# Kernel optimization log

Hardware: AMD Instinct MI355X
Metric: run time of the kernel (lower is better)

Reference implementation:

```python
import jax, jax.numpy as jnp
import numpy as np

N, FIN, C1, C2 = 4096, 6, 1000, 1000
K1, K2, KR = 3, 6, 3
NR, S, NCLS = 20, 205, 40


def pairwise_adj(x):
    # exp(-squared_euclidean_distance), RGCNN pairwise_distance
    inner = -2.0 * jnp.einsum('bnf,bmf->bnm', x, x)
    sq = jnp.sum(x * x, axis=-1, keepdims=True)
    return jnp.exp(-(sq + inner + jnp.swapaxes(sq, 1, 2)))


def knn_sparsify(adj, k):
    # keep top-k similarities per row, zero the rest (get_one_matrix_knn)
    vals, idx = jax.lax.top_k(adj, k)
    B, n, _ = adj.shape
    b = jnp.arange(B)[:, None, None]
    r = jnp.arange(n)[None, :, None]
    return jnp.zeros_like(adj).at[b, r, idx].set(vals)


def get_laplacian(W):
    # normalized Laplacian L = I - D^-1/2 W D^-1/2
    dinv = 1.0 / jnp.sqrt(jnp.sum(W, axis=-1))
    Lnorm = W * dinv[:, :, None] * dinv[:, None, :]
    return jnp.eye(W.shape[-1], dtype=W.dtype)[None] - Lnorm


def cheb_conv(x, L, W, b, K):
    # Chebyshev recursion: Tx0=x, Tx1=Lx, Txk=2L Tx_{k-1} - Tx_{k-2}
    Tx = [x]
    if K > 1:
        Tx.append(jnp.einsum('bnm,bmf->bnf', L, x))
    for _ in range(2, K):
        Tx.append(2.0 * jnp.einsum('bnm,bmf->bnf', L, Tx[-1]) - Tx[-2])
    xhat = jnp.concatenate(Tx, axis=-1)  # [B, N, K*Fin]
    return jnp.einsum('bnf,fo->bno', xhat, W) + b


def setup_inputs() -> dict:
    key = jax.random.key(0)
    ks = jax.random.split(key, 16)
    sc = 0.02
    return {
        'x': jax.random.normal(ks[0], (1, N, FIN), jnp.float32),
        'k': 40,
        'batch_size': 1,
        'num_points': N,
        'vertices_Reeb': jax.random.normal(ks[1], (NR, 3), jnp.float32),
        'laplacian_Reeb': jax.random.normal(ks[2], (NR, NR), jnp.float32),
        'sccs': jax.random.randint(ks[3], (NR, S), 0, N),
        'W1': jax.random.normal(ks[4], (K1 * FIN, C1), jnp.float32) * sc,
        'b1': jnp.zeros((C1,), jnp.float32),
        'W2': jax.random.normal(ks[5], (K2 * C1, C2), jnp.float32) * sc,
        'b2': jnp.zeros((C2,), jnp.float32),
        'Wr': jax.random.normal(ks[6], (KR * C1, C2), jnp.float32) * sc,
        'br': jnp.zeros((C2,), jnp.float32),
        'fc1_w': jax.random.normal(ks[7], (2 * C2, 512), jnp.float32) * sc,
        'fc1_b': jnp.zeros((512,), jnp.float32),
        'fc2_w': jax.random.normal(ks[8], (512, 128), jnp.float32) * sc,
        'fc2_b': jnp.zeros((128,), jnp.float32),
        'fc3_w': jax.random.normal(ks[9], (128, NCLS), jnp.float32) * sc,
        'fc3_b': jnp.zeros((NCLS,), jnp.float32),
    }


def reference(x, k, batch_size, num_points, vertices_Reeb, laplacian_Reeb, sccs,
              W1, b1, W2, b2, Wr, br, fc1_w, fc1_b, fc2_w, fc2_b, fc3_w, fc3_b):
    fro = lambda a: jnp.linalg.norm(a.reshape(-1))
    regs = []
    # dynamic KNN graph + Laplacian (no_grad in original -> stop_gradient)
    L = jax.lax.stop_gradient(get_laplacian(knn_sparsify(pairwise_adj(x), k)))
    out = jax.nn.relu(cheb_conv(x, L, W1, b1, K1))  # [1, N, 1000]
    regs.append(fro(jnp.einsum('bnc,bnm,bmf->bcf', out, L, x)))
    # Reeb pooling: max over each scc's node features (sample 0)
    vfr = jnp.max(out[0][sccs], axis=1)[None]  # [1, 20, 1000]
    L_reeb = laplacian_Reeb[None]
    # second dynamic graph on features
    L2 = jax.lax.stop_gradient(get_laplacian(knn_sparsify(pairwise_adj(out), k)))
    out2 = jax.nn.relu(cheb_conv(out, L2, W2, b2, K2))
    regs.append(fro(jnp.einsum('bnc,bnm,bmf->bcf', out2, L2, x)))
    out_reeb = jax.nn.relu(cheb_conv(vfr, L_reeb, Wr, br, KR))
    out_m = jnp.max(out2, axis=1)       # [1, 1000]
    reeb_m = jnp.max(out_reeb, axis=1)  # [1, 1000]
    of = jnp.concatenate([reeb_m, out_m], axis=1)  # [1, 2000]
    of = jax.nn.relu(of @ fc1_w + fc1_b)
    regs += [jnp.linalg.norm(fc1_w.T[0]) ** 2, fc1_b[0] ** 2]
    of = jax.nn.relu(of @ fc2_w + fc2_b)
    regs += [jnp.linalg.norm(fc2_w.T[0]) ** 2, fc2_b[0] ** 2]
    of = of @ fc3_w + fc3_b  # [1, 40]
    regs += [jnp.linalg.norm(fc3_w.T[0]) ** 2, fc3_b[0] ** 2]
    return of, jnp.stack(regs)
```

## Files before the change

### kernel.cpp

```cpp
#include <hip/hip_runtime.h>
#include <math.h>

#define N4    4096
#define FDIM  6
#define CC    1000
#define KP    1024
#define KP6   (6 * KP)
#define KNN   40
#define NRB   20
#define SSC   205

typedef __attribute__((ext_vector_type(8))) short bf16x8;
typedef __attribute__((ext_vector_type(4))) float f32x4;

__device__ __forceinline__ unsigned short f2bf(float f) {
    unsigned u = __float_as_uint(f);
    u = (u + 0x7fffu + ((u >> 16) & 1u)) >> 16;
    return (unsigned short)u;
}
__device__ __forceinline__ float bf2f(short s) {
    return __uint_as_float(((unsigned)(unsigned short)s) << 16);
}

__device__ __forceinline__ unsigned d2key(float d) {
    unsigned u = __float_as_uint(d);
    return ((int)u < 0) ? u : (~u) ^ 0x80000000u;
}
__device__ __forceinline__ float key2d(unsigned k) {
    unsigned u = (k >> 31) ? k : (~k) ^ 0x80000000u;
    return __uint_as_float(u);
}

__device__ __forceinline__ void gload16(const unsigned short* g, short* l) {
    __builtin_amdgcn_global_load_lds(
        (const __attribute__((address_space(1))) unsigned int*)g,
        (__attribute__((address_space(3))) unsigned int*)l, 16, 0, 0);
}


__global__ __launch_bounds__(256) void sqx_kernel(const float* __restrict__ x,
                                                  float* __restrict__ sq1,
                                                  float* __restrict__ xhat) {
    int n = blockIdx.x * blockDim.x + threadIdx.x;
    if (n >= N4) return;
    float s = 0.f;
#pragma unroll
    for (int f = 0; f < FDIM; ++f) {
        float v = x[n * FDIM + f];
        s += v * v;
        xhat[n * 18 + f] = v;
    }
    sq1[n] = s;
}


#define NHC 4
#define HSTRIDE 257

struct TopkSh {
    unsigned sv[N4];
    int hist[NHC * HSTRIDE];
    int sc[256];
    float red[8];
    unsigned short cidx[N4];
    unsigned short cv16[N4];
    unsigned s_pfx;
    int s_need, s_cnt, s_m;
};

__device__ __forceinline__ void topk_prep(TopkSh& sh, int t) {
    if (t == 0) { sh.s_pfx = 0u; sh.s_need = KNN; sh.s_cnt = 0; sh.s_m = 0; }
    for (int q = t; q < NHC * HSTRIDE; q += 512) sh.hist[q] = 0;
}

__device__ __forceinline__ void hist_pick(TopkSh& sh, int level, int t, int lane, int w, int nc) {
    if (t < 256) {
        int cnt = 0;
        for (int c = 0; c < nc; ++c) cnt += sh.hist[c * HSTRIDE + t];
        sh.sc[t] = cnt;
    }
    __syncthreads();
    if (w == 0) {
        int need = sh.s_need;
        unsigned pfx = sh.s_pfx;
        int c0 = sh.sc[4 * lane + 0], c1 = sh.sc[4 * lane + 1];
        int c2 = sh.sc[4 * lane + 2], c3 = sh.sc[4 * lane + 3];
        int s = c0 + c1 + c2 + c3;
        int suf = s;
#pragma unroll
        for (int off = 1; off < 64; off <<= 1) {
            int ov = __shfl_down(suf, off, 64);
            if (lane + off < 64) suf += ov;
        }
        int above = suf - s;
        int i3 = above + c3, i2 = i3 + c2, i1 = i2 + c1, i0 = i1 + c0;
        if (i3 >= need && i3 - c3 < need) { sh.s_need = need - (i3 - c3); sh.s_pfx = pfx | ((unsigned)(4 * lane + 3) << level); }
        if (i2 >= need && i2 - c2 < need) { sh.s_need = need - (i2 - c2); sh.s_pfx = pfx | ((unsigned)(4 * lane + 2) << level); }
        if (i1 >= need && i1 - c1 < need) { sh.s_need = need - (i1 - c1); sh.s_pfx = pfx | ((unsigned)(4 * lane + 1) << level); }
        if (i0 >= need && i0 - c0 < need) { sh.s_need = need - (i0 - c0); sh.s_pfx = pfx | ((unsigned)(4 * lane + 0) << level); }
    }
    __syncthreads();
}

template<int LASTLEVEL>
__device__ void topk_core(TopkSh& sh, int n, int* __restrict__ idx,
                          float* __restrict__ val, float* __restrict__ rowsum) {
    int t = threadIdx.x, lane = t & 63, w = t >> 6;
    __syncthreads();
    hist_pick(sh, 24, t, lane, w, NHC);
    unsigned b1 = sh.s_pfx >> 24;

    for (int i = t; i < N4; i += 512) {
        unsigned u = sh.sv[i];
        bool isc = ((u >> 24) >= b1);
        unsigned long long mm = __ballot(isc);
        int cw = __popcll(mm);
        int base = 0;
        if (lane == 0 && cw) base = atomicAdd(&sh.s_m, cw);
        base = __shfl(base, 0);
        if (isc) {
            int p = base + __popcll(mm & ((1ull << lane) - 1ull));
            sh.cidx[p] = (unsigned short)i;
            sh.cv16[p] = (unsigned short)(u >> 16);
        }
    }
    __syncthreads();
    int mcnt = sh.s_m;

    for (int q = t; q < HSTRIDE; q += 512) sh.hist[q] = 0;
    __syncthreads();
    {
        unsigned pb = sh.s_pfx >> 24;
        for (int j = t; j < mcnt; j += 512) {
            unsigned v = sh.cv16[j];
            if ((v >> 8) == pb) atomicAdd(&sh.hist[v & 255], 1);
        }
    }
    __syncthreads();
    hist_pick(sh, 16, t, lane, w, 1);

    if (LASTLEVEL == 0) {
        for (int q = t; q < HSTRIDE; q += 512) sh.hist[q] = 0;
        __syncthreads();
        {
            unsigned short p16 = (unsigned short)(sh.s_pfx >> 16);
            for (int j = t; j < mcnt; j += 512) {
                if (sh.cv16[j] == p16) {
                    unsigned u = sh.sv[sh.cidx[j]];
                    atomicAdd(&sh.hist[(u >> 8) & 255], 1);
                }
            }
        }
        __syncthreads();
        hist_pick(sh, 8, t, lane, w, 1);

        for (int q = t; q < HSTRIDE; q += 512) sh.hist[q] = 0;
        __syncthreads();
        {
            unsigned pfx = sh.s_pfx;
            unsigned short p16 = (unsigned short)(pfx >> 16);
            for (int j = t; j < mcnt; j += 512) {
                if (sh.cv16[j] == p16) {
                    unsigned u = sh.sv[sh.cidx[j]];
                    if ((u >> 8) == (pfx >> 8)) atomicAdd(&sh.hist[u & 255], 1);
                }
            }
        }
        __syncthreads();
        hist_pick(sh, 0, t, lane, w, 1);
    }

    unsigned Tbits = sh.s_pfx;
    if (LASTLEVEL == 16) Tbits |= (Tbits & 0x80000000u) ? 0u : 0xFFFFu;
    float Tf = __expf(-key2d(Tbits));
    int needEq = sh.s_need;

    float psum = 0.f;
    unsigned short T16 = (unsigned short)(Tbits >> 16);
    for (int j = t; j < mcnt; j += 512) {
        unsigned short v = sh.cv16[j];
        if (v >= T16) {
            unsigned u;
            if (LASTLEVEL == 16)
                u = ((unsigned)v << 16) | ((v & 0x8000u) ? 0u : 0xFFFFu);
            else
                u = sh.sv[sh.cidx[j]];
            if (u > Tbits) {
                int p = atomicAdd(&sh.s_cnt, 1);
                float fv = __expf(-key2d(u));
                idx[(size_t)n * KNN + p] = (int)sh.cidx[j];
                val[(size_t)n * KNN + p] = fv;
                psum += fv;
            }
        }
    }
#pragma unroll
    for (int o = 32; o; o >>= 1) psum += __shfl_down(psum, o);
    if (lane == 0) sh.red[w] = psum;
    __syncthreads();
    if (t == 0) {
        float s = 0.f;
#pragma unroll
        for (int q = 0; q < 8; ++q) s += sh.red[q];
        rowsum[n] = s + (float)needEq * Tf;
    }

    {
        int filled0 = KNN - needEq;
        int base_i = w * 512;
        int cnt = 0;
#pragma unroll
        for (int q = 0; q < 8; ++q) {
            bool eq = (sh.sv[base_i + q * 64 + lane] == Tbits);
            cnt += __popcll(__ballot(eq));
        }
        if (lane == 0) sh.sc[w] = cnt;
        __syncthreads();
        int pre = 0;
        for (int q = 0; q < w; ++q) pre += sh.sc[q];
        if (pre < needEq) {
            int run = pre;
            for (int q = 0; q < 8 && run < needEq; ++q) {
                bool eq = (sh.sv[base_i + q * 64 + lane] == Tbits);
                unsigned long long m = __ballot(eq);
                int lpre = __popcll(m & ((1ull << lane) - 1ull));
                if (eq && run + lpre < needEq) {
                    idx[(size_t)n * KNN + filled0 + run + lpre] = base_i + q * 64 + lane;
                    val[(size_t)n * KNN + filled0 + run + lpre] = Tf;
                }
                run += __popcll(m);
            }
        }
    }
}

__global__ __launch_bounds__(512) void topk_fused1(const float* __restrict__ x,
                                                   const float* __restrict__ sq1,
                                                   int* __restrict__ idx, float* __restrict__ val,
                                                   float* __restrict__ rowsum) {
    __shared__ TopkSh sh;
    __shared__ float xn[FDIM];
    __shared__ float sns;
    int n = blockIdx.x;
    int t = threadIdx.x;
    if (t < FDIM) xn[t] = x[n * FDIM + t];
    if (t == FDIM) sns = sq1[n];
    topk_prep(sh, t);
    __syncthreads();
    float x0 = xn[0], x1 = xn[1], x2 = xn[2], x3 = xn[3], x4 = xn[4], x5 = xn[5];
    float sn = sns;
    int* hw = &sh.hist[(t & 3) * HSTRIDE];
    unsigned prevb = 0xFFFFFFFFu; int rl = 0;
    for (int i = t; i < N4; i += 512) {
        const float2* xi = (const float2*)(x + i * FDIM);
        float2 p0 = xi[0], p1 = xi[1], p2 = xi[2];
        float d = x0 * p0.x + x1 * p0.y + x2 * p1.x + x3 * p1.y + x4 * p2.x + x5 * p2.y;
        float e = sn + sq1[i] - 2.f * d;
        unsigned k = d2key(e);
        sh.sv[i] = k;
        unsigned b = k >> 24;
        if (b == prevb) ++rl;
        else { if (rl) atomicAdd(&hw[prevb], rl); prevb = b; rl = 1; }
    }
    if (rl) atomicAdd(&hw[prevb], rl);
    topk_core<0>(sh, n, idx, val, rowsum);
}

__global__ __launch_bounds__(512) void topk_radix(const unsigned short* __restrict__ S,
                                                  int* __restrict__ idx, float* __restrict__ val,
                                                  float* __restrict__ rowsum) {
    __shared__ TopkSh sh;
    int n = blockIdx.x;
    int t = threadIdx.x;
    topk_prep(sh, t);
    const unsigned short* row = S + (size_t)n * N4;
    bf16x8 a = *(const bf16x8*)(row + 8 * t);
    __syncthreads();
    int* hw = &sh.hist[(t & 3) * HSTRIDE];
    unsigned prevb = 0xFFFFFFFFu; int rl = 0;
#pragma unroll
    for (int q = 0; q < 8; ++q) {
        unsigned k = d2key(bf2f(a[q]));
        sh.sv[8 * t + q] = k;
        unsigned b = k >> 24;
        if (b == prevb) ++rl;
        else { if (rl) atomicAdd(&hw[prevb], rl); prevb = b; rl = 1; }
    }
    if (rl) atomicAdd(&hw[prevb], rl);
    topk_core<16>(sh, n, idx, val, rowsum);
}

__global__ __launch_bounds__(256) void wnorm_kernel(float* __restrict__ wv,
                                                    const int* __restrict__ idx,
                                                    const float* __restrict__ rs) {
    int i = blockIdx.x * 256 + threadIdx.x;
    if (i >= N4 * KNN) return;
    int n = i / KNN;
    wv[i] = wv[i] * rsqrtf(rs[n]) * rsqrtf(rs[idx[i]]);
}

__global__ __launch_bounds__(64) void spmv_cheb(const float* __restrict__ Tc,
                                                const float* __restrict__ Tp,
                                                float* __restrict__ Tn,
                                                const int* __restrict__ idx,
                                                const float* __restrict__ wv,
                                                int F, int sC, int sP, int sN,
                                                float a, float b) {
    __shared__ int   si[KNN];
    __shared__ float sw[KNN];
    int n = blockIdx.x;
    if (threadIdx.x < KNN) {
        si[threadIdx.x] = idx[(size_t)n * KNN + threadIdx.x];
        sw[threadIdx.x] = wv[(size_t)n * KNN + threadIdx.x];
    }
    __syncthreads();
    for (int c = threadIdx.x; c < F; c += blockDim.x) {
        float s = 0.f;
#pragma unroll 8
        for (int j = 0; j < KNN; ++j) s += sw[j] * Tc[(size_t)si[j] * sC + c];
        float v = a * (Tc[(size_t)n * sC + c] - s);
        if (b != 0.f) v -= b * Tp[(size_t)n * sP + c];
        Tn[(size_t)n * sN + c] = v;
    }
}

__global__ __launch_bounds__(256) void spmv_cheb_bf(const unsigned short* __restrict__ Tcbf,
                                                    const unsigned short* __restrict__ Tpbf,
                                                    unsigned short* __restrict__ Tnbf,
                                                    const int* __restrict__ idx,
                                                    const float* __restrict__ wv,
                                                    float a, float b) {
    __shared__ int   si[KNN];
    __shared__ float sw[KNN];
    __shared__ float part[3][64][9];
    int n = blockIdx.x;
    int t = threadIdx.x;
    int tt = t & 63, g = t >> 6;
    if (t < KNN) {
        si[t] = idx[(size_t)n * KNN + t];
        sw[t] = wv[(size_t)n * KNN + t];
    }
    __syncthreads();
    int c = blockIdx.y * 512 + tt * 8;
    float acc0 = 0, acc1 = 0, acc2 = 0, acc3 = 0, acc4 = 0, acc5 = 0, acc6 = 0, acc7 = 0;
    int j0 = g * 10;
#pragma unroll
    for (int j = j0; j < j0 + 10; ++j) {
        bf16x8 v = *(const bf16x8*)(Tcbf + (size_t)si[j] * KP6 + c);
        float wj = sw[j];
        acc0 += wj * bf2f(v[0]); acc1 += wj * bf2f(v[1]);
        acc2 += wj * bf2f(v[2]); acc3 += wj * bf2f(v[3]);
        acc4 += wj * bf2f(v[4]); acc5 += wj * bf2f(v[5]);
        acc6 += wj * bf2f(v[6]); acc7 += wj * bf2f(v[7]);
    }
    if (g) {
        float* p = part[g - 1][tt];
        p[0] = acc0; p[1] = acc1; p[2] = acc2; p[3] = acc3;
        p[4] = acc4; p[5] = acc5; p[6] = acc6; p[7] = acc7;
    }
    __syncthreads();
    if (g == 0) {
#pragma unroll
        for (int pg = 0; pg < 3; ++pg) {
            const float* p = part[pg][tt];
            acc0 += p[0]; acc1 += p[1]; acc2 += p[2]; acc3 += p[3];
            acc4 += p[4]; acc5 += p[5]; acc6 += p[6]; acc7 += p[7];
        }
        bf16x8 tc = *(const bf16x8*)(Tcbf + (size_t)n * KP6 + c);
        float o0 = a * (bf2f(tc[0]) - acc0), o1 = a * (bf2f(tc[1]) - acc1);
        float o2 = a * (bf2f(tc[2]) - acc2), o3 = a * (bf2f(tc[3]) - acc3);
        float o4 = a * (bf2f(tc[4]) - acc4), o5 = a * (bf2f(tc[5]) - acc5);
        float o6 = a * (bf2f(tc[6]) - acc6), o7 = a * (bf2f(tc[7]) - acc7);
        if (b != 0.f) {
            bf16x8 tp = *(const bf16x8*)(Tpbf + (size_t)n * KP6 + c);
            o0 -= b * bf2f(tp[0]); o1 -= b * bf2f(tp[1]);
            o2 -= b * bf2f(tp[2]); o3 -= b * bf2f(tp[3]);
            o4 -= b * bf2f(tp[4]); o5 -= b * bf2f(tp[5]);
            o6 -= b * bf2f(tp[6]); o7 -= b * bf2f(tp[7]);
        }
        bf16x8 ob;
        ob[0] = (short)f2bf(o0); ob[1] = (short)f2bf(o1);
        ob[2] = (short)f2bf(o2); ob[3] = (short)f2bf(o3);
        ob[4] = (short)f2bf(o4); ob[5] = (short)f2bf(o5);
        ob[6] = (short)f2bf(o6); ob[7] = (short)f2bf(o7);
        *(bf16x8*)(Tnbf + (size_t)n * KP6 + c) = ob;
    }
}


__global__ __launch_bounds__(256) void cvt_bf16_kernel(const float* __restrict__ in,
                                                       unsigned short* __restrict__ out) {
    int i = blockIdx.x * 256 + threadIdx.x;
    int r = i >> 7, g = i & 127;
    bf16x8 v;
    if (g < 125) {
        float4 a = *(const float4*)(in + (size_t)r * CC + g * 8);
        float4 b = *(const float4*)(in + (size_t)r * CC + g * 8 + 4);
        v[0] = (short)f2bf(a.x); v[1] = (short)f2bf(a.y);
        v[2] = (short)f2bf(a.z); v[3] = (short)f2bf(a.w);
        v[4] = (short)f2bf(b.x); v[5] = (short)f2bf(b.y);
        v[6] = (short)f2bf(b.z); v[7] = (short)f2bf(b.w);
    } else {
#pragma unroll
        for (int q = 0; q < 8; ++q) v[q] = 0;
    }
    *(bf16x8*)(out + (size_t)r * KP6 + g * 8) = v;
}

__global__ __launch_bounds__(256) void w2t_kernel(const float* __restrict__ W2,
                                                  unsigned short* __restrict__ out) {
    __shared__ unsigned short tile[64][65];
    int t = threadIdx.x;
    int k0 = blockIdx.x * 64, n0 = blockIdx.y * 64, s = blockIdx.z;
#pragma unroll
    for (int p = 0; p < 16; ++p) {
        int i = p * 256 + t;
        int kk = i >> 6, nn = i & 63;
        int k = k0 + kk, n = n0 + nn;
        float v = (k < CC && n < CC) ? W2[((size_t)s * CC + k) * CC + n] : 0.f;
        tile[kk][nn] = f2bf(v);
    }
    __syncthreads();
#pragma unroll
    for (int p = 0; p < 16; ++p) {
        int i = p * 256 + t;
        int nn = i >> 6, kk = i & 63;
        out[(size_t)(n0 + nn) * KP6 + (size_t)s * KP + k0 + kk] = tile[kk][nn];
    }
}


#define LDT 32
#define SP2 136
#define SP 264
#define ABUF (128 * LDT)
#define BBUF (256 * LDT)

template<int STR>
__device__ __forceinline__ void gemm_core128_bk64(const unsigned short* __restrict__ Ag,
                                                  const unsigned short* __restrict__ Bg,
                                                  short* sm, int t,
                                                  int kbeg, int kend,
                                                  f32x4 (&acc)[4][4]) {
    int l = t & 63, w = t >> 6;
    int wm = (w >> 1) * 64, wn = (w & 1) * 64;
    int lr = l & 15, lq8 = (l >> 4) * 8;
    short* A0 = sm;
    short* A1 = sm + ABUF;
    short* B0 = sm + 2 * ABUF;
    short* B1 = sm + 3 * ABUF;
    size_t ga0 = (size_t)(32 * w + (l >> 2)) * STR + (l & 3) * 8;
    size_t ga1 = ga0 + (size_t)16 * STR;
    int lo = (32 * w) * LDT;
    for (int k0 = kbeg; k0 < kend; k0 += 64) {
        gload16(Ag + ga0 + k0,      A0 + lo);
        gload16(Ag + ga1 + k0,      A0 + lo + 16 * LDT);
        gload16(Ag + ga0 + k0 + 32, A1 + lo);
        gload16(Ag + ga1 + k0 + 32, A1 + lo + 16 * LDT);
        gload16(Bg + ga0 + k0,      B0 + lo);
        gload16(Bg + ga1 + k0,      B0 + lo + 16 * LDT);
        gload16(Bg + ga0 + k0 + 32, B1 + lo);
        gload16(Bg + ga1 + k0 + 32, B1 + lo + 16 * LDT);
        __syncthreads();
        bf16x8 af[4], bfr[4];
#pragma unroll
        for (int mi = 0; mi < 4; ++mi)
            af[mi] = *(const bf16x8*)&A0[(wm + mi * 16 + lr) * LDT + lq8];
#pragma unroll
        for (int ni = 0; ni < 4; ++ni)
            bfr[ni] = *(const bf16x8*)&B0[(wn + ni * 16 + lr) * LDT + lq8];
#pragma unroll
        for (int mi = 0; mi < 4; ++mi)
#pragma unroll
            for (int ni = 0; ni < 4; ++ni)
                acc[mi][ni] = __builtin_amdgcn_mfma_f32_16x16x32_bf16(af[mi], bfr[ni], acc[mi][ni], 0, 0, 0);
#pragma unroll
        for (int mi = 0; mi < 4; ++mi)
            af[mi] = *(const bf16x8*)&A1[(wm + mi * 16 + lr) * LDT + lq8];
#pragma unroll
        for (int ni = 0; ni < 4; ++ni)
            bfr[ni] = *(const bf16x8*)&B1[(wn + ni * 16 + lr) * LDT + lq8];
#pragma unroll
        for (int mi = 0; mi < 4; ++mi)
#pragma unroll
            for (int ni = 0; ni < 4; ++ni)
                acc[mi][ni] = __builtin_amdgcn_mfma_f32_16x16x32_bf16(af[mi], bfr[ni], acc[mi][ni], 0, 0, 0);
        __syncthreads();
    }
}

template<int STR>
__device__ __forceinline__ void gemm_core256(const unsigned short* __restrict__ Ag,
                                             const unsigned short* __restrict__ Bg,
                                             short* As, short* Bs, int t,
                                             int kbeg, int kend,
                                             f32x4 (&acc)[4][8]) {
    int l = t & 63, w = t >> 6;
    int wm = (w >> 1) * 64, wn = (w & 1) * 128;
    int lr = l & 15, lq8 = (l >> 4) * 8;
    size_t soff = (size_t)(16 * w + (l >> 2)) * STR + (l & 3) * 8;
    const unsigned short* gA = Ag + soff;
    const unsigned short* gB = Bg + soff;
    int wb = w * 512;
    gload16(gA + kbeg, As + wb);
    gload16(gA + kbeg + (size_t)64 * STR, As + wb + 64 * LDT);
    gload16(gB + kbeg, Bs + wb);
    gload16(gB + kbeg + (size_t)64 * STR, Bs + wb + 64 * LDT);
    gload16(gB + kbeg + (size_t)128 * STR, Bs + wb + 128 * LDT);
    gload16(gB + kbeg + (size_t)192 * STR, Bs + wb + 192 * LDT);
    __syncthreads();
    int cur = 0;
    for (int k0 = kbeg; k0 < kend; k0 += 32) {
        int nxt = cur ^ 1;
        if (k0 + 32 < kend) {
            short* nA = As + nxt * ABUF + wb;
            short* nB = Bs + nxt * BBUF + wb;
            gload16(gA + k0 + 32, nA);
            gload16(gA + k0 + 32 + (size_t)64 * STR, nA + 64 * LDT);
            gload16(gB + k0 + 32, nB);
            gload16(gB + k0 + 32 + (size_t)64 * STR, nB + 64 * LDT);
            gload16(gB + k0 + 32 + (size_t)128 * STR, nB + 128 * LDT);
            gload16(gB + k0 + 32 + (size_t)192 * STR, nB + 192 * LDT);
        }
        const short* cA = As + cur * ABUF;
        const short* cB = Bs + cur * BBUF;
        bf16x8 af[4], bfr[8];
#pragma unroll
        for (int mi = 0; mi < 4; ++mi)
            af[mi] = *(const bf16x8*)&cA[(wm + mi * 16 + lr) * LDT + lq8];
#pragma unroll
        for (int ni = 0; ni < 8; ++ni)
            bfr[ni] = *(const bf16x8*)&cB[(wn + ni * 16 + lr) * LDT + lq8];
#pragma unroll
        for (int mi = 0; mi < 4; ++mi)
#pragma unroll
            for (int ni = 0; ni < 8; ++ni)
                acc[mi][ni] = __builtin_amdgcn_mfma_f32_16x16x32_bf16(af[mi], bfr[ni], acc[mi][ni], 0, 0, 0);
        __syncthreads();
        cur = nxt;
    }
}

__global__ __launch_bounds__(256) void gemm_mfma_big(const unsigned short* __restrict__ A,
                                                     const unsigned short* __restrict__ B,
                                                     unsigned short* __restrict__ Cp) {
    __shared__ short smem[4 * ABUF];
    int t = threadIdx.x;
    int m0 = blockIdx.x * 128, n0 = blockIdx.y * 128;
    int kz = blockIdx.z;
    unsigned short* C = Cp + (size_t)kz * N4 * CC;
    f32x4 acc[4][4] = {};
    gemm_core128_bk64<KP6>(A + (size_t)m0 * KP6, B + (size_t)n0 * KP6, smem, t,
                           kz * 2 * KP, kz * 2 * KP + 2 * KP, acc);
    int l = t & 63, w = t >> 6;
    int wn = (w & 1) * 64;
    int lr = l & 15, lq4 = (l >> 4) * 4;
    int lrow = (w >> 1) * 16 + lq4;
#pragma unroll
    for (int mi = 0; mi < 4; ++mi) {
        __syncthreads();
#pragma unroll
        for (int ni = 0; ni < 4; ++ni) {
            int col = wn + ni * 16 + lr;
            f32x4 v = acc[mi][ni];
#pragma unroll
            for (int r = 0; r < 4; ++r) smem[(lrow + r) * SP2 + col] = (short)f2bf(v[r]);
        }
        __syncthreads();
#pragma unroll
        for (int q = 0; q < 2; ++q) {
            int row = q * 16 + (t >> 4);
            int col = (t & 15) * 8;
            int gm = m0 + (row >> 4) * 64 + mi * 16 + (row & 15);
            int gn = n0 + col;
            if (gn < CC) {
                bf16x8 vv = *(bf16x8*)&smem[row * SP2 + col];
                *(bf16x8*)(C + (size_t)gm * CC + gn) = vv;
            }
        }
    }
}

__global__ __launch_bounds__(256) void bias_relu_merge(const unsigned short* __restrict__ Cp,
                                                       const float* __restrict__ b2,
                                                       float* __restrict__ out2) {
    size_t i8 = (size_t)blockIdx.x * 256 + threadIdx.x;
    if (i8 >= (size_t)N4 * CC / 8) return;
    size_t i = i8 * 8;
    int c = (int)(i % CC);
    const size_t S = (size_t)N4 * CC;
    float s[8] = {};
#pragma unroll
    for (int z = 0; z < 3; ++z) {
        bf16x8 v = *(const bf16x8*)(Cp + z * S + i);
#pragma unroll
        for (int q = 0; q < 8; ++q) s[q] += bf2f(v[q]);
    }
    float4 o0, o1;
    o0.x = fmaxf(s[0] + b2[c + 0], 0.f); o0.y = fmaxf(s[1] + b2[c + 1], 0.f);
    o0.z = fmaxf(s[2] + b2[c + 2], 0.f); o0.w = fmaxf(s[3] + b2[c + 3], 0.f);
    o1.x = fmaxf(s[4] + b2[c + 4], 0.f); o1.y = fmaxf(s[5] + b2[c + 5], 0.f);
    o1.z = fmaxf(s[6] + b2[c + 6], 0.f); o1.w = fmaxf(s[7] + b2[c + 7], 0.f);
    *(float4*)(out2 + i) = o0;
    *(float4*)(out2 + i + 4) = o1;
}

__global__ __launch_bounds__(256, 2) void gram2_mfma(const unsigned short* __restrict__ Tall,
                                                     const float* __restrict__ sq2,
                                                     unsigned short* __restrict__ S) {
    __shared__ short smem[2 * ABUF + 2 * BBUF];
    short* As = smem;
    short* Bs = smem + 2 * ABUF;
    int t = threadIdx.x;
    int m0 = blockIdx.x * 128, n0 = blockIdx.y * 256;
    f32x4 acc[4][8] = {};
    gemm_core256<KP6>(Tall + (size_t)m0 * KP6, Tall + (size_t)n0 * KP6, As, Bs, t, 0, KP, acc);
    int l = t & 63, w = t >> 6;
    int wn = (w & 1) * 128;
    int lr = l & 15, lq4 = (l >> 4) * 4;
    int lrow = (w >> 1) * 16 + lq4;
#pragma unroll
    for (int mi = 0; mi < 4; ++mi) {
        __syncthreads();
        int mbase = m0 + (w >> 1) * 64 + mi * 16 + lq4;
#pragma unroll
        for (int ni = 0; ni < 8; ++ni) {
            int col = wn + ni * 16 + lr;
            float sn = sq2[n0 + col];
            f32x4 v = acc[mi][ni];
#pragma unroll
            for (int r = 0; r < 4; ++r)
                smem[(lrow + r) * SP + col] = (short)f2bf(sq2[mbase + r] + sn - 2.f * v[r]);
        }
        __syncthreads();
#pragma unroll
        for (int q = 0; q < 4; ++q) {
            int row = q * 8 + (t >> 5);
            int col = (t & 31) * 8;
            int gm = m0 + (row >> 4) * 64 + mi * 16 + (row & 15);
            int gn = n0 + col;
            bf16x8 vv = *(bf16x8*)&smem[row * SP + col];
            *(bf16x8*)(S + (size_t)gm * N4 + gn) = vv;
        }
    }
}


__global__ __launch_bounds__(256) void cheb1_out_kernel(const float* __restrict__ xhat,
                                                        const float* __restrict__ W1,
                                                        const float* __restrict__ b1,
                                                        float* __restrict__ outF) {
    __shared__ float xh[16][18];
    int n0 = blockIdx.x * 16;
    int tid = threadIdx.x;
    for (int i = tid; i < 16 * 18; i += 256) xh[i / 18][i % 18] = xhat[(size_t)n0 * 18 + i];
    __syncthreads();
    for (int c0 = 0; c0 < CC; c0 += 256) {
        int c = c0 + tid;
        if (c < CC) {
            float acc[16];
#pragma unroll
            for (int r = 0; r < 16; ++r) acc[r] = 0.f;
            for (int f = 0; f < 18; ++f) {
                float wv = W1[(size_t)f * CC + c];
#pragma unroll
                for (int r = 0; r < 16; ++r) acc[r] += xh[r][f] * wv;
            }
            float bb = b1[c];
#pragma unroll
            for (int r = 0; r < 16; ++r)
                outF[(size_t)(n0 + r) * CC + c] = fmaxf(acc[r] + bb, 0.f);
        }
    }
}


__global__ __launch_bounds__(256) void matT6_partial(const float* __restrict__ O,
                                                     const float* __restrict__ T, int ts,
                                                     float* __restrict__ M) {
    __shared__ float sT[128][6];
    int t = threadIdx.x;
    int c = blockIdx.x * 256 + t;
    int n0 = blockIdx.y * 128;
    for (int i = t; i < 128 * 6; i += 256) {
        int nn = i / 6, f = i % 6;
        sT[nn][f] = T[(size_t)(n0 + nn) * ts + f];
    }
    __syncthreads();
    if (c >= CC) return;
    float a0 = 0, a1 = 0, a2 = 0, a3 = 0, a4 = 0, a5 = 0;
    for (int nn = 0; nn < 128; ++nn) {
        float o = O[(size_t)(n0 + nn) * CC + c];
        a0 += o * sT[nn][0]; a1 += o * sT[nn][1]; a2 += o * sT[nn][2];
        a3 += o * sT[nn][3]; a4 += o * sT[nn][4]; a5 += o * sT[nn][5];
    }
    atomicAdd(&M[0 * CC + c], a0);
    atomicAdd(&M[1 * CC + c], a1);
    atomicAdd(&M[2 * CC + c], a2);
    atomicAdd(&M[3 * CC + c], a3);
    atomicAdd(&M[4 * CC + c], a4);
    atomicAdd(&M[5 * CC + c], a5);
}

__global__ __launch_bounds__(256) void fro_kernel(const float* __restrict__ M, float* __restrict__ dst) {
    __shared__ float red[256];
    int t = threadIdx.x;
    int i = blockIdx.x * 256 + t;
    float v = (i < 6 * CC) ? M[i] : 0.f;
    red[t] = v * v;
    __syncthreads();
    for (int o = 128; o; o >>= 1) { if (t < o) red[t] += red[t + o]; __syncthreads(); }
    if (t == 0) atomicAdd(dst, red[0]);
}


__global__ __launch_bounds__(256) void vfr_kernel(const float* __restrict__ outF,
                                                  const int* __restrict__ sccs,
                                                  float* __restrict__ vfr) {
    int r = blockIdx.y;
    int c = blockIdx.x * 256 + threadIdx.x;
    if (c >= CC) return;
    int s0 = blockIdx.z * 41;
    float m = 0.f;
    for (int s = s0; s < s0 + 41; ++s) {
        int n = sccs[r * SSC + s];
        m = fmaxf(m, outF[(size_t)n * CC + c]);
    }
    atomicMax((int*)&vfr[(size_t)r * CC + c], __float_as_int(m));
}

__global__ __launch_bounds__(256) void sq2_kernel(const float* __restrict__ outF,
                                                  float* __restrict__ sq2) {
    int lane = threadIdx.x & 63, w = threadIdx.x >> 6;
    int n = blockIdx.x * 4 + w;
    const float* row = outF + (size_t)n * CC;
    float s = 0.f;
    for (int i = lane; i < CC; i += 64) { float v = row[i]; s += v * v; }
#pragma unroll
    for (int o = 32; o; o >>= 1) s += __shfl_down(s, o);
    if (lane == 0) sq2[n] = s;
}

__global__ __launch_bounds__(256) void colmax_kernel(const float* __restrict__ O,
                                                     float* __restrict__ dst) {
    int c = blockIdx.x * 256 + threadIdx.x;
    if (c >= CC) return;
    int n0 = blockIdx.y * 64;
    float m = 0.f;
    for (int n = n0; n < n0 + 64; ++n) m = fmaxf(m, O[(size_t)n * CC + c]);
    atomicMax((int*)&dst[c], __float_as_int(m));
}


__global__ __launch_bounds__(256) void reeb_mm_kernel(const float* __restrict__ Lr,
                                                      const float* __restrict__ Vin,
                                                      const float* __restrict__ Vsub,
                                                      float* __restrict__ Vout, float a2) {
    int c = blockIdx.x * 256 + threadIdx.x;
    if (c >= CC) return;
    int r = blockIdx.y;
    float s = 0.f;
#pragma unroll
    for (int j = 0; j < NRB; ++j) s += Lr[r * NRB + j] * Vin[(size_t)j * CC + c];
    float v = a2 * s;
    if (Vsub) v -= Vsub[(size_t)r * CC + c];
    Vout[(size_t)r * CC + c] = v;
}

#define RKC 25
__global__ __launch_bounds__(256) void reeb_conv_splitk(const float* __restrict__ vfr,
                                                        const float* __restrict__ tr1,
                                                        const float* __restrict__ tr2,
                                                        const float* __restrict__ Wr,
                                                        float* __restrict__ rpre) {
    __shared__ float sA[NRB][RKC];
    int t = threadIdx.x;
    int kbase = blockIdx.y * RKC;
    for (int i = t; i < NRB * RKC; i += 256) {
        int r = i / RKC, kk = i % RKC;
        int kg = kbase + kk;
        float v;
        if (kg < CC)           v = vfr[(size_t)r * CC + kg];
        else if (kg < 2 * CC)  v = tr1[(size_t)r * CC + kg - CC];
        else                   v = tr2[(size_t)r * CC + kg - 2 * CC];
        sA[r][kk] = v;
    }
    __syncthreads();
    int c = blockIdx.x * 256 + t;
    if (c >= CC) return;
    float acc[NRB];
#pragma unroll
    for (int r = 0; r < NRB; ++r) acc[r] = 0.f;
    for (int kk = 0; kk < RKC; ++kk) {
        float wv = Wr[(size_t)(kbase + kk) * CC + c];
#pragma unroll
        for (int r = 0; r < NRB; ++r) acc[r] += sA[r][kk] * wv;
    }
#pragma unroll
    for (int r = 0; r < NRB; ++r) atomicAdd(&rpre[(size_t)r * CC + c], acc[r]);
}

__global__ __launch_bounds__(256) void reeb_max_kernel(const float* __restrict__ pre,
                                                       const float* __restrict__ br,
                                                       float* __restrict__ rbm) {
    int c = blockIdx.x * 256 + threadIdx.x;
    if (c >= CC) return;
    float bb = br[c];
    float m = 0.f;
    for (int r = 0; r < NRB; ++r) m = fmaxf(m, fmaxf(pre[(size_t)r * CC + c] + bb, 0.f));
    rbm[c] = m;
}


__global__ __launch_bounds__(256) void fc1_kernel(const float* __restrict__ rbm,
                                                  const float* __restrict__ otm,
                                                  const float* __restrict__ w,
                                                  float* __restrict__ h1pre) {
    int j = blockIdx.x * 256 + threadIdx.x;
    if (j >= 512) return;
    int i0 = blockIdx.y * 250;
    float s = 0.f;
    for (int i = i0; i < i0 + 250; ++i) {
        float v = (i < CC) ? rbm[i] : otm[i - CC];
        s += v * w[(size_t)i * 512 + j];
    }
    atomicAdd(&h1pre[j], s);
}

__global__ __launch_bounds__(512) void fc23_kernel(const float* __restrict__ h1pre,
                                                   const float* __restrict__ b1f,
                                                   const float* __restrict__ w2,
                                                   const float* __restrict__ b2f,
                                                   const float* __restrict__ w3,
                                                   const float* __restrict__ b3f,
                                                   float* __restrict__ dout) {
    __shared__ float h1[512];
    __shared__ float h2[128];
    int t = threadIdx.x;
    h1[t] = fmaxf(h1pre[t] + b1f[t], 0.f);
    __syncthreads();
    if (t < 128) {
        float s = b2f[t];
        for (int i = 0; i < 512; ++i) s += h1[i] * w2[(size_t)i * 128 + t];
        h2[t] = fmaxf(s, 0.f);
    }
    __syncthreads();
    if (t < 40) {
        float s = b3f[t];
        for (int i = 0; i < 128; ++i) s += h2[i] * w3[(size_t)i * 40 + t];
        dout[t] = s;
    }
}

__global__ __launch_bounds__(256) void finalize_kernel(const float* __restrict__ racc,
                                                       const float* __restrict__ f1w,
                                                       const float* __restrict__ f1b,
                                                       const float* __restrict__ f2w,
                                                       const float* __restrict__ f2b,
                                                       const float* __restrict__ f3w,
                                                       const float* __restrict__ f3b,
                                                       float* __restrict__ dout) {
    __shared__ float red[256];
    __shared__ float res[3];
    int t = threadIdx.x;
    float s1 = 0.f, s2 = 0.f, s3 = 0.f;
    for (int i = t; i < 2000; i += 256) { float v = f1w[(size_t)i * 512]; s1 += v * v; }
    for (int i = t; i < 512; i += 256) { float v = f2w[(size_t)i * 128]; s2 += v * v; }
    if (t < 128) { float v = f3w[(size_t)t * 40]; s3 = v * v; }

    red[t] = s1; __syncthreads();
    for (int o = 128; o; o >>= 1) { if (t < o) red[t] += red[t + o]; __syncthreads(); }
    if (t == 0) res[0] = red[0];
    __syncthreads();
    red[t] = s2; __syncthreads();
    for (int o = 128; o; o >>= 1) { if (t < o) red[t] += red[t + o]; __syncthreads(); }
    if (t == 0) res[1] = red[0];
    __syncthreads();
    red[t] = s3; __syncthreads();
    for (int o = 128; o; o >>= 1) { if (t < o) red[t] += red[t + o]; __syncthreads(); }
    if (t == 0) res[2] = red[0];
    __syncthreads();

    if (t == 0) {
        dout[40] = sqrtf(racc[0]);
        dout[41] = sqrtf(racc[1]);
        dout[42] = res[0];
        dout[43] = f1b[0] * f1b[0];
        dout[44] = res[1];
        dout[45] = f2b[0] * f2b[0];
        dout[46] = res[2];
        dout[47] = f3b[0] * f3b[0];
    }
}


extern "C" void kernel_launch(void* const* d_in, const int* in_sizes, int n_in,
                              void* d_out, int out_size, void* d_ws, size_t ws_size,
                              hipStream_t stream) {
    const float* x    = (const float*)d_in[0];
    const float* Lr   = (const float*)d_in[5];
    const int*   sccs = (const int*)d_in[6];
    const float* W1   = (const float*)d_in[7];
    const float* b1   = (const float*)d_in[8];
    const float* W2   = (const float*)d_in[9];
    const float* b2   = (const float*)d_in[10];
    const float* Wr   = (const float*)d_in[11];
    const float* br   = (const float*)d_in[12];
    const float* f1w  = (const float*)d_in[13];
    const float* f1b  = (const float*)d_in[14];
    const float* f2w  = (const float*)d_in[15];
    const float* f2b  = (const float*)d_in[16];
    const float* f3w  = (const float*)d_in[17];
    const float* f3b  = (const float*)d_in[18];
    float* dout = (float*)d_out;

    char* ws = (char*)d_ws;
    size_t off = 0;
    auto alloc = [&](size_t bytes) -> char* {
        char* p = ws + off;
        off = (off + bytes + 255) & ~(size_t)255;
        return p;
    };
    float* outF = (float*)alloc((size_t)N4 * CC * 4);
    unsigned short* Cpb = (unsigned short*)alloc((size_t)6 * N4 * CC * 2);
    unsigned short* Sb  = (unsigned short*)alloc((size_t)N4 * N4 * 2);
    unsigned short* Tall = (unsigned short*)alloc((size_t)N4 * KP6 * 2);
    unsigned short* W2T6 = Sb;
    float* xhat = (float*)alloc((size_t)N4 * 18 * 4);
    float* sq1  = (float*)alloc(N4 * 4);
    float* sq2  = (float*)alloc(N4 * 4);
    float* rs1  = (float*)alloc(N4 * 4);
    float* rs2  = (float*)alloc(N4 * 4);
    float* wv1  = (float*)alloc((size_t)N4 * KNN * 4);
    float* wv2  = (float*)alloc((size_t)N4 * KNN * 4);
    int*   ix1  = (int*)alloc((size_t)N4 * KNN * 4);
    int*   ix2  = (int*)alloc((size_t)N4 * KNN * 4);
    float* t2x  = (float*)alloc((size_t)N4 * FDIM * 4);
    float* tr1  = (float*)alloc((size_t)NRB * CC * 4);
    float* tr2  = (float*)alloc((size_t)NRB * CC * 4);
    char*  zbase = ws + off;
    float* Mb   = (float*)alloc(6 * CC * 4);
    float* Mb2  = (float*)alloc(6 * CC * 4);
    float* rbm  = (float*)alloc(CC * 4);
    float* otm  = (float*)alloc(CC * 4);
    float* h1p  = (float*)alloc(512 * 4);
    float* racc = (float*)alloc(64 * 4);
    float* rpre = (float*)alloc((size_t)NRB * CC * 4);
    float* vfr  = (float*)alloc((size_t)NRB * CC * 4);
    size_t zlen = (size_t)((ws + off) - zbase);
    if (off > ws_size) return;

    hipMemsetAsync(zbase, 0, zlen, stream);

    sqx_kernel<<<(N4 + 255) / 256, 256, 0, stream>>>(x, sq1, xhat);
    topk_fused1<<<N4, 512, 0, stream>>>(x, sq1, ix1, wv1, rs1);
    wnorm_kernel<<<(N4 * KNN + 255) / 256, 256, 0, stream>>>(wv1, ix1, rs1);

    spmv_cheb<<<N4, 64, 0, stream>>>(xhat, xhat, xhat + 6, ix1, wv1, FDIM, 18, 18, 18, 1.f, 0.f);
    spmv_cheb<<<N4, 64, 0, stream>>>(xhat + 6, xhat, xhat + 12, ix1, wv1, FDIM, 18, 18, 18, 2.f, 1.f);
    cheb1_out_kernel<<<N4 / 16, 256, 0, stream>>>(xhat, W1, b1, outF);

    matT6_partial<<<dim3(4, 32), 256, 0, stream>>>(outF, xhat + 6, 18, Mb);
    fro_kernel<<<24, 256, 0, stream>>>(Mb, racc + 0);

    vfr_kernel<<<dim3(4, NRB, 5), 256, 0, stream>>>(outF, sccs, vfr);

    sq2_kernel<<<N4 / 4, 256, 0, stream>>>(outF, sq2);
    cvt_bf16_kernel<<<N4 * 128 / 256, 256, 0, stream>>>(outF, Tall);
    gram2_mfma<<<dim3(N4 / 128, N4 / 256), 256, 0, stream>>>(Tall, sq2, Sb);
    topk_radix<<<N4, 512, 0, stream>>>(Sb, ix2, wv2, rs2);
    wnorm_kernel<<<(N4 * KNN + 255) / 256, 256, 0, stream>>>(wv2, ix2, rs2);

    w2t_kernel<<<dim3(16, 16, 6), 256, 0, stream>>>(W2, W2T6);

    spmv_cheb<<<N4, 64, 0, stream>>>(x, x, t2x, ix2, wv2, FDIM, FDIM, FDIM, FDIM, 1.f, 0.f);

    spmv_cheb_bf<<<dim3(N4, 2), 256, 0, stream>>>(Tall + 0 * KP, Tall + 0 * KP, Tall + 1 * KP, ix2, wv2, 1.f, 0.f);
    spmv_cheb_bf<<<dim3(N4, 2), 256, 0, stream>>>(Tall + 1 * KP, Tall + 0 * KP, Tall + 2 * KP, ix2, wv2, 2.f, 1.f);
    spmv_cheb_bf<<<dim3(N4, 2), 256, 0, stream>>>(Tall + 2 * KP, Tall + 1 * KP, Tall + 3 * KP, ix2, wv2, 2.f, 1.f);
    spmv_cheb_bf<<<dim3(N4, 2), 256, 0, stream>>>(Tall + 3 * KP, Tall + 2 * KP, Tall + 4 * KP, ix2, wv2, 2.f, 1.f);
    spmv_cheb_bf<<<dim3(N4, 2), 256, 0, stream>>>(Tall + 4 * KP, Tall + 3 * KP, Tall + 5 * KP, ix2, wv2, 2.f, 1.f);

    gemm_mfma_big<<<dim3(N4 / 128, 8, 3), 256, 0, stream>>>(Tall, W2T6, Cpb);
    bias_relu_merge<<<(int)(((size_t)N4 * CC / 8 + 255) / 256), 256, 0, stream>>>(Cpb, b2, outF);

    matT6_partial<<<dim3(4, 32), 256, 0, stream>>>(outF, t2x, FDIM, Mb2);
    fro_kernel<<<24, 256, 0, stream>>>(Mb2, racc + 1);

    colmax_kernel<<<dim3(4, 64), 256, 0, stream>>>(outF, otm);

    reeb_mm_kernel<<<dim3(4, NRB), 256, 0, stream>>>(Lr, vfr, nullptr, tr1, 1.f);
    reeb_mm_kernel<<<dim3(4, NRB), 256, 0, stream>>>(Lr, tr1, vfr, tr2, 2.f);
    reeb_conv_splitk<<<dim3(4, 120), 256, 0, stream>>>(vfr, tr1, tr2, Wr, rpre);
    reeb_max_kernel<<<4, 256, 0, stream>>>(rpre, br, rbm);

    fc1_kernel<<<dim3(2, 8), 256, 0, stream>>>(rbm, otm, f1w, h1p);
    fc23_kernel<<<1, 512, 0, stream>>>(h1p, f1b, f2w, f2b, f3w, f3b, dout);
    finalize_kernel<<<1, 256, 0, stream>>>(racc, f1w, f1b, f2w, f2b, f3w, f3b, dout);
}
```

Before: 604.6 us.

## Enlarge big GEMM tiles to 256x256 with 512 threads and split-K of four

The main MFMA GEMM moves from 128x128 tiles with 4 waves and a 3-way K split to 256x256 tiles with 8 waves and a 4-way K split. Each wave now computes 128x64 instead of 64x64. The goal is more operand reuse per byte loaded and fewer blocks. The merge kernel now sums four partial bf16 slices, which adds memory traffic and needs a larger partial buffer. The smaller grid may also leave the GPU less fully occupied.

Result: slower. 618.8 us (+2.3%).

```diff
diff --git a/kernel.cpp b/kernel.cpp
--- a/kernel.cpp
+++ b/kernel.cpp
@@ -435,59 +435,6 @@
 #define SP 264
 #define ABUF (128 * LDT)
 #define BBUF (256 * LDT)
-
-template<int STR>
-__device__ __forceinline__ void gemm_core128_bk64(const unsigned short* __restrict__ Ag,
-                                                  const unsigned short* __restrict__ Bg,
-                                                  short* sm, int t,
-                                                  int kbeg, int kend,
-                                                  f32x4 (&acc)[4][4]) {
-    int l = t & 63, w = t >> 6;
-    int wm = (w >> 1) * 64, wn = (w & 1) * 64;
-    int lr = l & 15, lq8 = (l >> 4) * 8;
-    short* A0 = sm;
-    short* A1 = sm + ABUF;
-    short* B0 = sm + 2 * ABUF;
-    short* B1 = sm + 3 * ABUF;
-    size_t ga0 = (size_t)(32 * w + (l >> 2)) * STR + (l & 3) * 8;
-    size_t ga1 = ga0 + (size_t)16 * STR;
-    int lo = (32 * w) * LDT;
-    for (int k0 = kbeg; k0 < kend; k0 += 64) {
-        gload16(Ag + ga0 + k0,      A0 + lo);
-        gload16(Ag + ga1 + k0,      A0 + lo + 16 * LDT);
-        gload16(Ag + ga0 + k0 + 32, A1 + lo);
-        gload16(Ag + ga1 + k0 + 32, A1 + lo + 16 * LDT);
-        gload16(Bg + ga0 + k0,      B0 + lo);
-        gload16(Bg + ga1 + k0,      B0 + lo + 16 * LDT);
-        gload16(Bg + ga0 + k0 + 32, B1 + lo);
-        gload16(Bg + ga1 + k0 + 32, B1 + lo + 16 * LDT);
-        __syncthreads();
-        bf16x8 af[4], bfr[4];
-#pragma unroll
-        for (int mi = 0; mi < 4; ++mi)
-            af[mi] = *(const bf16x8*)&A0[(wm + mi * 16 + lr) * LDT + lq8];
-#pragma unroll
-        for (int ni = 0; ni < 4; ++ni)
-            bfr[ni] = *(const bf16x8*)&B0[(wn + ni * 16 + lr) * LDT + lq8];
-#pragma unroll
-        for (int mi = 0; mi < 4; ++mi)
-#pragma unroll
-            for (int ni = 0; ni < 4; ++ni)
-                acc[mi][ni] = __builtin_amdgcn_mfma_f32_16x16x32_bf16(af[mi], bfr[ni], acc[mi][ni], 0, 0, 0);
-#pragma unroll
-        for (int mi = 0; mi < 4; ++mi)
-            af[mi] = *(const bf16x8*)&A1[(wm + mi * 16 + lr) * LDT + lq8];
-#pragma unroll
-        for (int ni = 0; ni < 4; ++ni)
-            bfr[ni] = *(const bf16x8*)&B1[(wn + ni * 16 + lr) * LDT + lq8];
-#pragma unroll
-        for (int mi = 0; mi < 4; ++mi)
-#pragma unroll
-            for (int ni = 0; ni < 4; ++ni)
-                acc[mi][ni] = __builtin_amdgcn_mfma_f32_16x16x32_bf16(af[mi], bfr[ni], acc[mi][ni], 0, 0, 0);
-        __syncthreads();
-    }
-}
 
 template<int STR>
 __device__ __forceinline__ void gemm_core256(const unsigned short* __restrict__ Ag,
@@ -541,40 +488,84 @@
     }
 }
 
-__global__ __launch_bounds__(256) void gemm_mfma_big(const unsigned short* __restrict__ A,
-                                                     const unsigned short* __restrict__ B,
-                                                     unsigned short* __restrict__ Cp) {
-    __shared__ short smem[4 * ABUF];
-    int t = threadIdx.x;
-    int m0 = blockIdx.x * 128, n0 = blockIdx.y * 128;
+__global__ __launch_bounds__(512, 2) void gemm_mfma_big(const unsigned short* __restrict__ A,
+                                                        const unsigned short* __restrict__ B,
+                                                        unsigned short* __restrict__ Cp) {
+    __shared__ short smem[4 * BBUF];
+    int t = threadIdx.x;
+    int m0 = blockIdx.x * 256, n0 = blockIdx.y * 256;
     int kz = blockIdx.z;
     unsigned short* C = Cp + (size_t)kz * N4 * CC;
-    f32x4 acc[4][4] = {};
-    gemm_core128_bk64<KP6>(A + (size_t)m0 * KP6, B + (size_t)n0 * KP6, smem, t,
-                           kz * 2 * KP, kz * 2 * KP + 2 * KP, acc);
+    f32x4 acc[8][4] = {};
     int l = t & 63, w = t >> 6;
-    int wn = (w & 1) * 64;
-    int lr = l & 15, lq4 = (l >> 4) * 4;
-    int lrow = (w >> 1) * 16 + lq4;
-#pragma unroll
-    for (int mi = 0; mi < 4; ++mi) {
+    int wm = (w >> 2) * 128, wn = (w & 3) * 64;
+    int lr = l & 15, lq8 = (l >> 4) * 8;
+    short* A0 = smem;
+    short* A1 = smem + BBUF;
+    short* B0 = smem + 2 * BBUF;
+    short* B1 = smem + 3 * BBUF;
+    const unsigned short* Ag = A + (size_t)m0 * KP6;
+    const unsigned short* Bg = B + (size_t)n0 * KP6;
+    size_t ga = (size_t)(32 * w + (l >> 2)) * KP6 + (l & 3) * 8;
+    int lo = (32 * w) * LDT;
+    int kbeg = kz * 1536, kend = kbeg + 1536;
+    for (int k0 = kbeg; k0 < kend; k0 += 64) {
+        gload16(Ag + ga + k0,                         A0 + lo);
+        gload16(Ag + ga + (size_t)16 * KP6 + k0,      A0 + lo + 16 * LDT);
+        gload16(Ag + ga + k0 + 32,                    A1 + lo);
+        gload16(Ag + ga + (size_t)16 * KP6 + k0 + 32, A1 + lo + 16 * LDT);
+        gload16(Bg + ga + k0,                         B0 + lo);
+        gload16(Bg + ga + (size_t)16 * KP6 + k0,      B0 + lo + 16 * LDT);
+        gload16(Bg + ga + k0 + 32,                    B1 + lo);
+        gload16(Bg + ga + (size_t)16 * KP6 + k0 + 32, B1 + lo + 16 * LDT);
+        __syncthreads();
+        bf16x8 af[8], bfr[4];
+#pragma unroll
+        for (int mi = 0; mi < 8; ++mi)
+            af[mi] = *(const bf16x8*)&A0[(wm + mi * 16 + lr) * LDT + lq8];
+#pragma unroll
+        for (int ni = 0; ni < 4; ++ni)
+            bfr[ni] = *(const bf16x8*)&B0[(wn + ni * 16 + lr) * LDT + lq8];
+#pragma unroll
+        for (int mi = 0; mi < 8; ++mi)
+#pragma unroll
+            for (int ni = 0; ni < 4; ++ni)
+                acc[mi][ni] = __builtin_amdgcn_mfma_f32_16x16x32_bf16(af[mi], bfr[ni], acc[mi][ni], 0, 0, 0);
+#pragma unroll
+        for (int mi = 0; mi < 8; ++mi)
+            af[mi] = *(const bf16x8*)&A1[(wm + mi * 16 + lr) * LDT + lq8];
+#pragma unroll
+        for (int ni = 0; ni < 4; ++ni)
+            bfr[ni] = *(const bf16x8*)&B1[(wn + ni * 16 + lr) * LDT + lq8];
+#pragma unroll
+        for (int mi = 0; mi < 8; ++mi)
+#pragma unroll
+            for (int ni = 0; ni < 4; ++ni)
+                acc[mi][ni] = __builtin_amdgcn_mfma_f32_16x16x32_bf16(af[mi], bfr[ni], acc[mi][ni], 0, 0, 0);
+        __syncthreads();
+    }
+    int lq4 = (l >> 4) * 4;
+#pragma unroll
+    for (int mi = 0; mi < 8; ++mi) {
         __syncthreads();
 #pragma unroll
         for (int ni = 0; ni < 4; ++ni) {
             int col = wn + ni * 16 + lr;
             f32x4 v = acc[mi][ni];
 #pragma unroll
-            for (int r = 0; r < 4; ++r) smem[(lrow + r) * SP2 + col] = (short)f2bf(v[r]);
+            for (int r = 0; r < 4; ++r)
+                smem[((w >> 2) * 16 + lq4 + r) * SP + col] = (short)f2bf(v[r]);
         }
         __syncthreads();
 #pragma unroll
         for (int q = 0; q < 2; ++q) {
-            int row = q * 16 + (t >> 4);
-            int col = (t & 15) * 8;
-            int gm = m0 + (row >> 4) * 64 + mi * 16 + (row & 15);
+            int i = q * 512 + t;
+            int row = i >> 5;
+            int col = (i & 31) * 8;
+            int gm = m0 + (row >> 4) * 128 + mi * 16 + (row & 15);
             int gn = n0 + col;
             if (gn < CC) {
-                bf16x8 vv = *(bf16x8*)&smem[row * SP2 + col];
+                bf16x8 vv = *(bf16x8*)&smem[row * SP + col];
                 *(bf16x8*)(C + (size_t)gm * CC + gn) = vv;
             }
         }
@@ -591,7 +582,7 @@
     const size_t S = (size_t)N4 * CC;
     float s[8] = {};
 #pragma unroll
-    for (int z = 0; z < 3; ++z) {
+    for (int z = 0; z < 4; ++z) {
         bf16x8 v = *(const bf16x8*)(Cp + z * S + i);
 #pragma unroll
         for (int q = 0; q < 8; ++q) s[q] += bf2f(v[q]);
@@ -981,7 +972,7 @@
     spmv_cheb_bf<<<dim3(N4, 2), 256, 0, stream>>>(Tall + 3 * KP, Tall + 2 * KP, Tall + 4 * KP, ix2, wv2, 2.f, 1.f);
     spmv_cheb_bf<<<dim3(N4, 2), 256, 0, stream>>>(Tall + 4 * KP, Tall + 3 * KP, Tall + 5 * KP, ix2, wv2, 2.f, 1.f);
 
-    gemm_mfma_big<<<dim3(N4 / 128, 8, 3), 256, 0, stream>>>(Tall, W2T6, Cpb);
+    gemm_mfma_big<<<dim3(N4 / 256, 4, 4), 512, 0, stream>>>(Tall, W2T6, Cpb);
     bias_relu_merge<<<(int)(((size_t)N4 * CC / 8 + 255) / 256), 256, 0, stream>>>(Cpb, b2, outF);
 
     matT6_partial<<<dim3(4, 32), 256, 0, stream>>>(outF, t2x, FDIM, Mb2);
```
